# Optimization experiments

Hardware: AMD Instinct MI355X
Metric: run time of the kernel (lower is better)

## Reference

```python
import jax, jax.numpy as jnp
import numpy as np

D_MODEL = 96
D_STATE = 16
D_INNER = 192   # expand * d_model
DT_RANK = 6     # ceil(96/16)
D_DEPTH_OUT = 1024  # (64/2)*(64/2)
BATCH, HH, WW = 2, 64, 64


def silu(v):
    return v * jax.nn.sigmoid(v)


def setup_inputs() -> dict:
    key = jax.random.key(0)
    ks = jax.random.split(key, 10)
    f = jnp.float32
    x = jax.random.normal(ks[0], (BATCH, HH, WW, D_MODEL), f)
    in_proj_w = jax.random.normal(ks[1], (2 * D_INNER, D_MODEL), f) * 0.02
    conv2d_w = jax.random.normal(ks[2], (D_INNER, 1, 3, 3), f) * 0.1  # depthwise, groups=D_INNER
    conv2d_b = jnp.zeros((D_INNER,), f)
    depth_conv_w = jax.random.normal(ks[3], (D_INNER, 1, 3, 3), f) * 0.1  # depthwise, stride 2
    depth_conv_b = jnp.zeros((D_INNER,), f)
    depth_fc_w = jax.random.normal(ks[4], (D_INNER, D_DEPTH_OUT), f) * 0.02
    depth_fc_b = jnp.zeros((D_INNER,), f)
    x_proj_w = jax.random.normal(ks[5], (DT_RANK + 2 * D_STATE, D_INNER), f) * 0.02
    dt_init_std = DT_RANK ** (-0.5)
    dt_projs_w = jax.random.uniform(ks[6], (D_INNER, DT_RANK), f, -dt_init_std, dt_init_std)
    # inverse-softplus of dt ~ U(log 1e-3, log 0.1)
    dt = jnp.exp(jax.random.uniform(ks[7], (D_INNER,), f) * (np.log(0.1) - np.log(0.001)) + np.log(0.001))
    dt = jnp.clip(dt, 1e-4, None)
    dt_projs_b = dt + jnp.log(-jnp.expm1(-dt))
    A_logs = jnp.log(jnp.tile(jnp.arange(1, D_STATE + 1, dtype=f)[None, :], (D_INNER, 1)))
    Ds = jnp.ones((D_INNER,), f)
    out_norm_w = jnp.ones((D_INNER,), f)
    out_norm_b = jnp.zeros((D_INNER,), f)
    out_proj_w = jax.random.normal(ks[8], (D_MODEL, D_INNER), f) * 0.02
    return dict(x=x, in_proj_w=in_proj_w, conv2d_w=conv2d_w, conv2d_b=conv2d_b,
                depth_conv_w=depth_conv_w, depth_conv_b=depth_conv_b,
                depth_fc_w=depth_fc_w, depth_fc_b=depth_fc_b, x_proj_w=x_proj_w,
                dt_projs_w=dt_projs_w, dt_projs_b=dt_projs_b, A_logs=A_logs, Ds=Ds,
                out_norm_w=out_norm_w, out_norm_b=out_norm_b, out_proj_w=out_proj_w)


def _selective_scan(u, delta, A, Bm, Cm, D, delta_bias):
    # u, delta: [B, D, L]; A: [D, N]; Bm, Cm: [B, N, L]; D: [D]; delta_bias: [D]
    delta = jax.nn.softplus(delta + delta_bias[None, :, None])
    dA = jnp.exp(jnp.einsum('bdl,dn->lbdn', delta, A))          # [L,B,D,N]
    dBu = jnp.einsum('bdl,bnl,bdl->lbdn', delta, Bm, u)          # [L,B,D,N]
    Ct = jnp.transpose(Cm, (2, 0, 1))                            # [L,B,N]
    h0 = jnp.zeros(dA.shape[1:], u.dtype)

    def step(h, inp):
        a, b, c = inp
        h = a * h + b                                            # S6 recurrence
        return h, jnp.einsum('bdn,bn->bd', h, c)

    _, ys = jax.lax.scan(step, h0, (dA, dBu, Ct))                # ys: [L,B,D]
    y = jnp.transpose(ys, (1, 2, 0))                             # [B,D,L]
    return y + D[None, :, None] * u


def _forward(x, in_proj_w, conv2d_w, conv2d_b, depth_conv_w, depth_conv_b,
             depth_fc_w, depth_fc_b, x_proj_w, dt_projs_w, dt_projs_b,
             A_logs, Ds, out_norm_w, out_norm_b, out_proj_w):
    B, H, W, _ = x.shape
    Di, N, R = D_INNER, D_STATE, DT_RANK
    dn = ('NCHW', 'OIHW', 'NCHW')
    xz = x @ in_proj_w.T
    x1, z = jnp.split(xz, 2, axis=-1)
    xc = jnp.transpose(x1, (0, 3, 1, 2))                         # [B,Di,H,W]
    xc = jax.lax.conv_general_dilated(xc, conv2d_w, (1, 1), [(1, 1), (1, 1)],
                                      dimension_numbers=dn, feature_group_count=Di)
    xc = silu(xc + conv2d_b[None, :, None, None])
    dxc = jax.lax.conv_general_dilated(xc, depth_conv_w, (2, 2), [(1, 1), (1, 1)],
                                       dimension_numbers=dn, feature_group_count=Di)
    dxc = dxc + depth_conv_b[None, :, None, None]                # [B,Di,H/2,W/2]
    dx = dxc.reshape(B, Di, -1)                                  # [B,Di,1024]
    dx = dx @ depth_fc_w.T + depth_fc_b                          # [B,Di,Di]
    dx = silu(jnp.transpose(dx, (0, 2, 1)))                      # [B,Di,CC], CC=Di
    L = H * W
    CC = dx.shape[-1]
    xs = jnp.concatenate([dx, xc.reshape(B, Di, L)], axis=-1)    # mode='head': [B,Di,LL]
    x_dbl = jnp.einsum('bdl,cd->bcl', xs, x_proj_w)
    dts, Bm, Cm = x_dbl[:, :R], x_dbl[:, R:R + N], x_dbl[:, R + N:]
    dts = jnp.einsum('brl,dr->bdl', dts, dt_projs_w)
    A = -jnp.exp(A_logs)
    y = _selective_scan(xs, dts, A, Bm, Cm, Ds, dt_projs_b)
    y = y[..., CC:]                                              # drop depth tokens (head mode)
    y = jnp.transpose(y, (0, 2, 1)).reshape(B, H, W, Di)
    mu = jnp.mean(y, axis=-1, keepdims=True)
    var = jnp.var(y, axis=-1, keepdims=True)
    y = (y - mu) * jax.lax.rsqrt(var + 1e-5) * out_norm_w + out_norm_b
    y = y * silu(z)
    return y @ out_proj_w.T


def reference(x, in_proj_w, conv2d_w, conv2d_b, depth_conv_w, depth_conv_b,
              depth_fc_w, depth_fc_b, x_proj_w, dt_projs_w, dt_projs_b,
              A_logs, Ds, out_norm_w, out_norm_b, out_proj_w):
    return _forward(x, in_proj_w, conv2d_w, conv2d_b, depth_conv_w, depth_conv_b,
                    depth_fc_w, depth_fc_b, x_proj_w, dt_projs_w, dt_projs_b,
                    A_logs, Ds, out_norm_w, out_norm_b, out_proj_w)
```

## Files before the change

### kernel.cpp

```cpp
#include <hip/hip_runtime.h>
#include <hip/hip_bf16.h>

typedef __hip_bfloat16 bf16;

#define BATCH 2
#define DM 96
#define DI 192
#define LSP 4096
#define LD 192
#define LTOT 4288
#define NST 16
#define RK 6
#define DFC 1024
#define CLEN 64
#define NCH 67
#define SCH 64
#define XR 16
#define NG  (BATCH * DI * NST)

__device__ __forceinline__ float b2f(bf16 v) { return __bfloat162float(v); }
__device__ __forceinline__ float silu_f(float x) { return x / (1.f + __expf(-x)); }
__device__ __forceinline__ float softplus_f(float x) { return x > 20.f ? x : log1pf(__expf(x)); }

__device__ __forceinline__ int is_f32(const void* alog) {
    return ((const unsigned int*)alog)[0] == 0u;
}
__device__ __forceinline__ float LDI(const void* p, int i, int f32m) {
    return f32m ? ((const float*)p)[i] : __bfloat162float(((const bf16*)p)[i]);
}
__device__ __forceinline__ void unpack2(unsigned int u, float* o) {
    o[0] = __uint_as_float(u << 16);
    o[1] = __uint_as_float(u & 0xffff0000u);
}

__global__ __launch_bounds__(768) void k_inproj(const void* __restrict__ x, const void* __restrict__ ipw,
                                                const void* __restrict__ alog,
                                                float* __restrict__ x1, float* __restrict__ z) {
    __shared__ uint4 sxr[384];
    const int f32m = is_f32(alog);
    int t = threadIdx.x;
    int col = t >> 1;
    int kh = t & 1;
    int row0 = blockIdx.x * 16;
    float wr[48];
    if (f32m) {
        const float4* wp = (const float4*)((const float*)ipw + col * 96 + kh * 48);
        #pragma unroll
        for (int i = 0; i < 12; i++) {
            float4 v = wp[i];
            wr[4*i] = v.x; wr[4*i+1] = v.y; wr[4*i+2] = v.z; wr[4*i+3] = v.w;
        }
        if (t < 384) sxr[t] = ((const uint4*)((const float*)x + row0 * 96))[t];
        __syncthreads();
        for (int r = 0; r < 16; r++) {
            const uint4* xr = &sxr[r * 24 + kh * 12];
            float acc = 0.f;
            #pragma unroll
            for (int i = 0; i < 12; i++) {
                uint4 u = xr[i];
                acc += __uint_as_float(u.x) * wr[4*i]   + __uint_as_float(u.y) * wr[4*i+1]
                     + __uint_as_float(u.z) * wr[4*i+2] + __uint_as_float(u.w) * wr[4*i+3];
            }
            acc += __shfl_xor(acc, 1);
            if (kh == 0) {
                int row = row0 + r;
                if (col < DI) x1[row * DI + col] = acc;
                else          z[row * DI + (col - DI)] = acc;
            }
        }
    } else {
        const uint4* wp = (const uint4*)((const bf16*)ipw + col * 96 + kh * 48);
        #pragma unroll
        for (int i = 0; i < 6; i++) {
            uint4 v = wp[i];
            unpack2(v.x, &wr[8*i]);   unpack2(v.y, &wr[8*i+2]);
            unpack2(v.z, &wr[8*i+4]); unpack2(v.w, &wr[8*i+6]);
        }
        if (t < 192) sxr[t] = ((const uint4*)((const bf16*)x + row0 * 96))[t];
        __syncthreads();
        for (int r = 0; r < 16; r++) {
            const uint4* xr = &sxr[r * 12 + kh * 6];
            float acc = 0.f;
            #pragma unroll
            for (int i = 0; i < 6; i++) {
                uint4 xv = xr[i];
                float xf8[8];
                unpack2(xv.x, &xf8[0]); unpack2(xv.y, &xf8[2]);
                unpack2(xv.z, &xf8[4]); unpack2(xv.w, &xf8[6]);
                #pragma unroll
                for (int j = 0; j < 8; j++) acc += xf8[j] * wr[8*i + j];
            }
            acc += __shfl_xor(acc, 1);
            if (kh == 0) {
                int row = row0 + r;
                if (col < DI) x1[row * DI + col] = acc;
                else          z[row * DI + (col - DI)] = acc;
            }
        }
    }
}

__global__ __launch_bounds__(192) void k_conv1(const float* __restrict__ x1, const void* __restrict__ cw,
                                               const void* __restrict__ cb, float* __restrict__ xs,
                                               const void* __restrict__ alog) {
    const int f32m = is_f32(alog);
    int d = threadIdx.x;
    int blk = blockIdx.x;
    int b = blk >> 9;
    int rest = blk & 511;
    int h = rest >> 3, w0 = (rest & 7) * 8;
    float wgt[9];
    #pragma unroll
    for (int i = 0; i < 9; i++) wgt[i] = LDI(cw, d * 9 + i, f32m);
    float bias = LDI(cb, d, f32m);
    float val[3][10];
    #pragma unroll
    for (int dh = 0; dh < 3; dh++) {
        int hh = h + dh - 1;
        #pragma unroll
        for (int j = 0; j < 10; j++) {
            int ww = w0 + j - 1;
            val[dh][j] = ((unsigned)hh < 64u && (unsigned)ww < 64u)
                       ? x1[((b << 12) + (hh << 6) + ww) * DI + d] : 0.f;
        }
    }
    #pragma unroll
    for (int i = 0; i < 8; i++) {
        float acc = bias;
        #pragma unroll
        for (int dh = 0; dh < 3; dh++)
            #pragma unroll
            for (int dw = 0; dw < 3; dw++)
                acc += val[dh][i + dw] * wgt[dh * 3 + dw];
        xs[(b * LTOT + LD + (h << 6) + w0 + i) * DI + d] = silu_f(acc);
    }
}

__global__ __launch_bounds__(192) void k_conv2(const float* __restrict__ xs, const void* __restrict__ dw,
                                               const void* __restrict__ db, float* __restrict__ dxc,
                                               const void* __restrict__ alog) {
    const int f32m = is_f32(alog);
    int d = threadIdx.x;
    int blk = blockIdx.x;
    int b = blk >> 10, lp = blk & 1023;
    int hp = lp >> 5, wp = lp & 31;
    float acc = LDI(db, d, f32m);
    #pragma unroll
    for (int dh = 0; dh < 3; dh++) {
        int h = 2 * hp + dh - 1;
        if ((unsigned)h >= 64u) continue;
        #pragma unroll
        for (int dw_ = 0; dw_ < 3; dw_++) {
            int w_ = 2 * wp + dw_ - 1;
            if ((unsigned)w_ >= 64u) continue;
            acc += xs[(b * LTOT + LD + (h << 6) + w_) * DI + d] * LDI(dw, d * 9 + dh * 3 + dw_, f32m);
        }
    }
    dxc[(b * DFC + lp) * DI + d] = acc;
}

__global__ __launch_bounds__(192) void k_dfc(const float* __restrict__ dxc, const void* __restrict__ fw,
                                             float* __restrict__ part, const void* __restrict__ alog) {
    __shared__ float sfw[4 * 128];
    const int f32m = is_f32(alog);
    int t = threadIdx.x;
    int blk = blockIdx.x;
    int p = blk / 96;
    int rem = blk - p * 96;
    int b   = rem / 48;
    int ch0 = (rem % 48) * 4;
    int k0  = p * 128;
    for (int idx = t; idx < 4 * 128; idx += 192)
        sfw[idx] = LDI(fw, (ch0 + (idx >> 7)) * DFC + k0 + (idx & 127), f32m);
    __syncthreads();
    float a0 = 0.f, a1 = 0.f, a2 = 0.f, a3 = 0.f;
    #pragma unroll 8
    for (int k = 0; k < 128; k++) {
        float dv = dxc[(b * DFC + k0 + k) * DI + t];
        a0 += dv * sfw[k];
        a1 += dv * sfw[128 + k];
        a2 += dv * sfw[256 + k];
        a3 += dv * sfw[384 + k];
    }
    int ob = ((p * 2 + b) * 192 + t) * DI + ch0;
    *(float4*)&part[ob] = make_float4(a0, a1, a2, a3);
}

__global__ __launch_bounds__(256) void k_xdbl(const float* __restrict__ xs_r, float* __restrict__ xs_w,
                                              const float* __restrict__ part, const void* __restrict__ fb,
                                              const void* __restrict__ xpw,
                                              float* __restrict__ BCb, float* __restrict__ dts,
                                              const void* __restrict__ alog) {
    __shared__ float sw[38 * 196];
    __shared__ float srow[XR][196];
    const int f32m = is_f32(alog);
    int t = threadIdx.x;
    for (int c = t >> 3; c < 38; c += 32) {
        int seg = (t & 7) * 24;
        for (int k = seg; k < seg + 24; k++) sw[c * 196 + k] = LDI(xpw, c * DI + k, f32m);
    }
    int row0 = blockIdx.x * XR;
    int bb = row0 >= LTOT ? 1 : 0;
    int depth = (row0 - bb * LTOT) < LD;
    for (int idx = t; idx < XR * DI; idx += 256) {
        int row = idx / DI, k = idx - row * DI;
        int grow = row0 + row;
        float v;
        if (depth) {
            int tok = grow - bb * LTOT;
            int o = (bb * 192 + tok) * DI + k;
            v = 0.f;
            #pragma unroll
            for (int p = 0; p < 8; p++) v += part[o + p * 73728];
            v = silu_f(v + LDI(fb, k, f32m));
            xs_w[grow * DI + k] = v;
        } else {
            v = xs_r[grow * DI + k];
        }
        srow[row][k] = v;
    }
    __syncthreads();
    int r = t & 15, cg = t >> 4;
    float a0 = 0.f, a1 = 0.f, a2 = 0.f;
    const float4* w0 = (const float4*)&sw[cg * 196];
    const float4* w1 = (const float4*)&sw[(cg + 16) * 196];
    const float4* w2 = (const float4*)&sw[(cg < 6 ? cg + 32 : cg) * 196];
    const float4* xr = (const float4*)&srow[r][0];
    #pragma unroll 4
    for (int k = 0; k < 48; k++) {
        float4 xv = xr[k], v0 = w0[k], v1 = w1[k], v2 = w2[k];
        a0 += xv.x * v0.x + xv.y * v0.y + xv.z * v0.z + xv.w * v0.w;
        a1 += xv.x * v1.x + xv.y * v1.y + xv.z * v1.z + xv.w * v1.w;
        a2 += xv.x * v2.x + xv.y * v2.y + xv.z * v2.z + xv.w * v2.w;
    }
    int grow = row0 + r;
    if (cg < 6) dts[grow * 6 + cg] = a0;
    else        BCb[grow * 32 + (cg - 6)] = a0;
    BCb[grow * 32 + (cg + 10)] = a1;
    if (cg < 6) BCb[grow * 32 + (cg + 26)] = a2;
}

__device__ __forceinline__ void delta_block(const float* sdts, const float* sdwb, float* sdel, int t) {
    int e = t * 4;
    int i = e >> 4, dl = e & 15;
    #pragma unroll
    for (int q = 0; q < 4; q++) {
        int dlq = dl + q;
        float dv = sdwb[96 + dlq];
        #pragma unroll
        for (int r2 = 0; r2 < RK; r2++) dv += sdts[i * RK + r2] * sdwb[dlq * RK + r2];
        sdel[e + q] = softplus_f(dv);
    }
}

__global__ __launch_bounds__(256) void k_scan1(const float* __restrict__ dts, const float* __restrict__ xs,
                                               const float* __restrict__ BCb, const void* __restrict__ dtw,
                                               const void* __restrict__ dtb, const void* __restrict__ alog,
                                               float2* __restrict__ AH) {
    __shared__ float su[CLEN * 16];
    __shared__ float sB[CLEN * 16];
    __shared__ float sdel[CLEN * 16];
    __shared__ float sdts[CLEN * RK];
    __shared__ float sdwb[112];
    const int f32m = is_f32(alog);
    int t = threadIdx.x;
    int beta = blockIdx.x;
    int b = beta / (12 * NCH);
    int rem = beta - b * (12 * NCH);
    int dblk = rem / NCH, ch = rem - dblk * NCH;
    int d0 = dblk * 16, l0 = ch * CLEN;
    int bL = b * LTOT;
    {
        int e = t * 4;
        int i = e >> 4, dd = e & 15;
        *(float4*)&su[e] = *(const float4*)&xs[(bL + l0 + i) * DI + d0 + dd];
        *(float4*)&sB[e] = *(const float4*)&BCb[(bL + l0 + i) * 32 + dd];
    }
    for (int idx = t; idx < CLEN * RK; idx += 256) sdts[idx] = dts[(bL + l0) * RK + idx];
    if (t < 96)            sdwb[t] = LDI(dtw, (d0 + t / 6) * RK + (t % 6), f32m);
    else if (t < 112)      sdwb[t] = LDI(dtb, d0 + (t - 96), f32m);
    __syncthreads();
    delta_block(sdts, sdwb, sdel, t);
    __syncthreads();
    int dloc = t >> 4, n = t & 15;
    int d = d0 + dloc;
    float A = -__expf(LDI(alog, d * NST + n, f32m));
    float h = 0.f, ap = 1.f;
    #pragma unroll 4
    for (int i = 0; i < CLEN; i++) {
        float dt = sdel[(i << 4) | dloc];
        float u  = su[(i << 4) | dloc];
        float Bv = sB[(i << 4) | n];
        float a = __expf(dt * A);
        h = a * h + dt * Bv * u;
        ap *= a;
    }
    int g = ((b * DI + d) * NST) + n;
    AH[ch * NG + g] = make_float2(ap, h);
}

__global__ __launch_bounds__(64) void k_scan2(const float2* __restrict__ AH, float* __restrict__ He) {
    int g = blockIdx.x * 64 + threadIdx.x;
    float h = 0.f;
    for (int ch = 0; ch < NCH; ch++) {
        He[ch * NG + g] = h;
        float2 v = AH[ch * NG + g];
        h = v.x * h + v.y;
    }
}

__global__ __launch_bounds__(256) void k_scan3(const float* __restrict__ dts, const float* __restrict__ xs,
                                               const float* __restrict__ BCb, const void* __restrict__ dtw,
                                               const void* __restrict__ dtb, const void* __restrict__ alog,
                                               const void* __restrict__ Dsv, const float* __restrict__ He,
                                               float* __restrict__ y) {
    __shared__ float su[CLEN * 16];
    __shared__ float sbc[CLEN * 32];
    __shared__ float sdel[CLEN * 16];
    __shared__ float sdts[CLEN * RK];
    __shared__ float sdwb[112];
    const int f32m = is_f32(alog);
    int t = threadIdx.x;
    int beta = blockIdx.x;
    int b = beta / (12 * SCH);
    int rem = beta - b * (12 * SCH);
    int dblk = rem / SCH, ch = (rem - dblk * SCH) + 3;
    int d0 = dblk * 16, l0 = ch * CLEN;
    int bL = b * LTOT;
    {
        int e = t * 4;
        int i = e >> 4, dd = e & 15;
        *(float4*)&su[e] = *(const float4*)&xs[(bL + l0 + i) * DI + d0 + dd];
    }
    #pragma unroll
    for (int q = 0; q < 2; q++) {
        int e = (t + q * 256) * 4;
        int i = e >> 5, c = e & 31;
        *(float4*)&sbc[e] = *(const float4*)&BCb[(bL + l0 + i) * 32 + c];
    }
    for (int idx = t; idx < CLEN * RK; idx += 256) sdts[idx] = dts[(bL + l0) * RK + idx];
    if (t < 96)            sdwb[t] = LDI(dtw, (d0 + t / 6) * RK + (t % 6), f32m);
    else if (t < 112)      sdwb[t] = LDI(dtb, d0 + (t - 96), f32m);
    __syncthreads();
    delta_block(sdts, sdwb, sdel, t);
    __syncthreads();
    int dloc = t >> 4, n = t & 15;
    int d = d0 + dloc;
    float A = -__expf(LDI(alog, d * NST + n, f32m));
    float Dv = LDI(Dsv, d, f32m);
    int g = ((b * DI + d) * NST) + n;
    float h = He[ch * NG + g];
    for (int i = 0; i < CLEN; i++) {
        float dt = sdel[(i << 4) | dloc];
        float u  = su[(i << 4) | dloc];
        float Bv = sbc[(i << 5) | n];
        float Cv = sbc[(i << 5) | 16 | n];
        float a = __expf(dt * A);
        h = a * h + dt * Bv * u;
        float yv = h * Cv;
        #pragma unroll
        for (int m = 8; m; m >>= 1) yv += __shfl_xor(yv, m, 16);
        int l = l0 + i;
        if (n == 0) y[(b * LSP + (l - LD)) * DI + d] = yv + Dv * u;
    }
}

__global__ __launch_bounds__(384) void k_out(const float* __restrict__ y, const float* __restrict__ z,
                                             const void* __restrict__ nw, const void* __restrict__ nb,
                                             const void* __restrict__ opw, void* __restrict__ out,
                                             const void* __restrict__ alog) {
    __shared__ float sg[2][DI];
    __shared__ float sred[2][2][3];
    const int f32m = is_f32(alog);
    int t = threadIdx.x;
    int m = t >> 2, kh = t & 3;
    float wr[48];
    if (f32m) {
        const float4* wp = (const float4*)((const float*)opw + m * DI + kh * 48);
        #pragma unroll
        for (int i = 0; i < 12; i++) {
            float4 v = wp[i];
            wr[4*i] = v.x; wr[4*i+1] = v.y; wr[4*i+2] = v.z; wr[4*i+3] = v.w;
        }
    } else {
        const uint4* wp = (const uint4*)((const bf16*)opw + m * DI + kh * 48);
        #pragma unroll
        for (int i = 0; i < 6; i++) {
            uint4 v = wp[i];
            unpack2(v.x, &wr[8*i]);   unpack2(v.y, &wr[8*i+2]);
            unpack2(v.z, &wr[8*i+4]); unpack2(v.w, &wr[8*i+6]);
        }
    }
    float nwv = 0.f, nbv = 0.f;
    if (t < DI) { nwv = LDI(nw, t, f32m); nbv = LDI(nb, t, f32m); }
    int wv_ = t >> 6;
    int row0 = blockIdx.x * 16;
    for (int pr = 0; pr < 8; pr++) {
        int r0 = row0 + pr * 2, r1 = r0 + 1;
        float y0 = 0.f, z0 = 0.f, y1 = 0.f, z1 = 0.f;
        if (t < DI) {
            y0 = y[r0 * DI + t]; z0 = z[r0 * DI + t];
            y1 = y[r1 * DI + t]; z1 = z[r1 * DI + t];
            float s0 = y0, q0 = y0 * y0, s1 = y1, q1 = y1 * y1;
            #pragma unroll
            for (int off = 32; off; off >>= 1) {
                s0 += __shfl_xor(s0, off); q0 += __shfl_xor(q0, off);
                s1 += __shfl_xor(s1, off); q1 += __shfl_xor(q1, off);
            }
            if ((t & 63) == 0) {
                sred[0][0][wv_] = s0; sred[0][1][wv_] = q0;
                sred[1][0][wv_] = s1; sred[1][1][wv_] = q1;
            }
        }
        __syncthreads();
        if (t < DI) {
            float S0  = sred[0][0][0] + sred[0][0][1] + sred[0][0][2];
            float Q0  = sred[0][1][0] + sred[0][1][1] + sred[0][1][2];
            float S1  = sred[1][0][0] + sred[1][0][1] + sred[1][0][2];
            float Q1  = sred[1][1][0] + sred[1][1][1] + sred[1][1][2];
            float mu0 = S0 * (1.f / 192.f), var0 = Q0 * (1.f / 192.f) - mu0 * mu0;
            float mu1 = S1 * (1.f / 192.f), var1 = Q1 * (1.f / 192.f) - mu1 * mu1;
            float g0 = (y0 - mu0) * rsqrtf(var0 + 1e-5f) * nwv + nbv;
            g0 *= z0 / (1.f + __expf(-z0));
            float g1 = (y1 - mu1) * rsqrtf(var1 + 1e-5f) * nwv + nbv;
            g1 *= z1 / (1.f + __expf(-z1));
            sg[0][t] = g0;
            sg[1][t] = g1;
        }
        __syncthreads();
        const float* g0p = &sg[0][kh * 48];
        const float* g1p = &sg[1][kh * 48];
        float a0 = 0.f, a1 = 0.f;
        #pragma unroll
        for (int j = 0; j < 48; j++) {
            a0 += g0p[j] * wr[j];
            a1 += g1p[j] * wr[j];
        }
        a0 += __shfl_xor(a0, 1); a0 += __shfl_xor(a0, 2);
        a1 += __shfl_xor(a1, 1); a1 += __shfl_xor(a1, 2);
        if (kh == 0) {
            if (f32m) {
                ((float*)out)[r0 * DM + m] = a0;
                ((float*)out)[r1 * DM + m] = a1;
            } else {
                ((bf16*)out)[r0 * DM + m] = __float2bfloat16(a0);
                ((bf16*)out)[r1 * DM + m] = __float2bfloat16(a1);
            }
        }
    }
}

extern "C" void kernel_launch(void* const* d_in, const int* in_sizes, int n_in,
                              void* d_out, int out_size, void* d_ws, size_t ws_size,
                              hipStream_t stream) {
    (void)in_sizes; (void)n_in; (void)out_size; (void)ws_size;
    const void* x    = d_in[0];
    const void* ipw  = d_in[1];
    const void* c1w  = d_in[2];
    const void* c1b  = d_in[3];
    const void* c2w  = d_in[4];
    const void* c2b  = d_in[5];
    const void* fcw  = d_in[6];
    const void* fcb  = d_in[7];
    const void* xpw  = d_in[8];
    const void* dtw  = d_in[9];
    const void* dtb  = d_in[10];
    const void* alog = d_in[11];
    const void* Dsv  = d_in[12];
    const void* nw   = d_in[13];
    const void* nb   = d_in[14];
    const void* opw  = d_in[15];

    float* ws  = (float*)d_ws;
    float* x1  = ws;
    float* z   = x1  + BATCH * LSP * DI;
    float* xs  = z   + BATCH * LSP * DI;
    float* dxc = xs  + BATCH * LTOT * DI;
    float* BCb = dxc + BATCH * DFC * DI;
    float* dts = BCb + BATCH * LTOT * 32;
    float2* AH = (float2*)(dts + BATCH * LTOT * RK);
    float* He  = (float*)(AH + NCH * NG);
    float* part = x1;
    float* y    = x1;

    k_inproj<<<dim3(512), dim3(768), 0, stream>>>(x, ipw, alog, x1, z);
    k_conv1 <<<dim3(1024), dim3(DI), 0, stream>>>(x1, c1w, c1b, xs, alog);
    k_conv2 <<<dim3(BATCH * DFC), dim3(DI), 0, stream>>>(xs, c2w, c2b, dxc, alog);
    k_dfc   <<<dim3(768), dim3(DI), 0, stream>>>(dxc, fcw, part, alog);
    k_xdbl  <<<dim3(536), dim3(256), 0, stream>>>(xs, xs, part, fcb, xpw, BCb, dts, alog);
    k_scan1 <<<dim3(BATCH * 12 * NCH), dim3(256), 0, stream>>>(dts, xs, BCb, dtw, dtb, alog, AH);
    k_scan2 <<<dim3(96), dim3(64), 0, stream>>>(AH, He);
    k_scan3 <<<dim3(BATCH * 12 * SCH), dim3(256), 0, stream>>>(dts, xs, BCb, dtw, dtb, alog, Dsv, He, y);
    k_out   <<<dim3(512), dim3(384), 0, stream>>>(y, z, nw, nb, opw, d_out, alog);
}
```

Before: 223.6 us.

## Transpose scan shared-memory tiles, use DPP reductions, register-tile the input projection

The input projection is rewritten as a 4x4 register-tiled GEMM. A new prep kernel transposes the projection weight each call so that weight reads are coalesced float4 loads. In both scan kernels, delta, u, B and C are stored in shared memory transposed with a rotating swizzle, so each thread reads four timesteps with one float4 load without bank conflicts. The scan3 output reduction over 16 lanes switches from shfl_xor to DPP row operations. The extra launch and the scattered shared-memory stores during the load phase add some overhead.

```diff
diff --git a/kernel.cpp b/kernel.cpp
--- a/kernel.cpp
+++ b/kernel.cpp
@@ -33,70 +33,81 @@
     o[1] = __uint_as_float(u & 0xffff0000u);
 }
 
-__global__ __launch_bounds__(768) void k_inproj(const void* __restrict__ x, const void* __restrict__ ipw,
-                                                const void* __restrict__ alog,
-                                                float* __restrict__ x1, float* __restrict__ z) {
-    __shared__ uint4 sxr[384];
+__device__ __forceinline__ float row16_sum(float v) {
+    v += __int_as_float(__builtin_amdgcn_update_dpp(0, __float_as_int(v), 0x128, 0xf, 0xf, true));
+    v += __int_as_float(__builtin_amdgcn_update_dpp(0, __float_as_int(v), 0x124, 0xf, 0xf, true));
+    v += __int_as_float(__builtin_amdgcn_update_dpp(0, __float_as_int(v), 0x122, 0xf, 0xf, true));
+    v += __int_as_float(__builtin_amdgcn_update_dpp(0, __float_as_int(v), 0x121, 0xf, 0xf, true));
+    return v;
+}
+
+#define TW(r, i)  ((r) * 64 + ((((i) >> 2) + (r)) & 15) * 4 + ((i) & 3))
+
+__global__ __launch_bounds__(256) void k_wprep(const void* __restrict__ ipw, float* __restrict__ wT,
+                                               const void* __restrict__ alog) {
+    const int f32m = is_f32(alog);
+    int idx = blockIdx.x * 256 + threadIdx.x;
+    if (idx < 96 * 384) {
+        int k = idx / 384, c = idx - k * 384;
+        wT[idx] = LDI(ipw, c * 96 + k, f32m);
+    }
+}
+
+__global__ __launch_bounds__(384) void k_inproj2(const void* __restrict__ x, const float* __restrict__ wT,
+                                                 float* __restrict__ x1, float* __restrict__ z,
+                                                 const void* __restrict__ alog) {
+    __shared__ __align__(16) float sx[16 * 100];
     const int f32m = is_f32(alog);
     int t = threadIdx.x;
-    int col = t >> 1;
-    int kh = t & 1;
     int row0 = blockIdx.x * 16;
-    float wr[48];
-    if (f32m) {
-        const float4* wp = (const float4*)((const float*)ipw + col * 96 + kh * 48);
-        #pragma unroll
-        for (int i = 0; i < 12; i++) {
-            float4 v = wp[i];
-            wr[4*i] = v.x; wr[4*i+1] = v.y; wr[4*i+2] = v.z; wr[4*i+3] = v.w;
-        }
-        if (t < 384) sxr[t] = ((const uint4*)((const float*)x + row0 * 96))[t];
-        __syncthreads();
-        for (int r = 0; r < 16; r++) {
-            const uint4* xr = &sxr[r * 24 + kh * 12];
-            float acc = 0.f;
+    {
+        int e = t * 4;
+        int row = e / 96, k = e - row * 96;
+        float4 v;
+        if (f32m) {
+            v = *((const float4*)((const float*)x + (row0 + row) * 96 + k));
+        } else {
+            uint2 u = *((const uint2*)((const ushort*)x + (row0 + row) * 96 + k));
+            float f[4];
+            unpack2(u.x, &f[0]); unpack2(u.y, &f[2]);
+            v = make_float4(f[0], f[1], f[2], f[3]);
+        }
+        *(float4*)&sx[row * 100 + k] = v;
+    }
+    __syncthreads();
+    int rg = t / 96, cg = t - rg * 96;
+    int c0 = cg * 4, rbase = rg * 4;
+    float acc[4][4];
+    #pragma unroll
+    for (int r = 0; r < 4; r++)
+        #pragma unroll
+        for (int cc = 0; cc < 4; cc++) acc[r][cc] = 0.f;
+    const float* wp = wT + c0;
+    #pragma unroll 4
+    for (int k4 = 0; k4 < 24; k4++) {
+        float4 xv[4], wv[4];
+        #pragma unroll
+        for (int r = 0; r < 4; r++) xv[r] = *(const float4*)&sx[(rbase + r) * 100 + k4 * 4];
+        #pragma unroll
+        for (int q = 0; q < 4; q++) wv[q] = *(const float4*)&wp[(k4 * 4 + q) * 384];
+        #pragma unroll
+        for (int r = 0; r < 4; r++) {
+            float xr[4] = {xv[r].x, xv[r].y, xv[r].z, xv[r].w};
             #pragma unroll
-            for (int i = 0; i < 12; i++) {
-                uint4 u = xr[i];
-                acc += __uint_as_float(u.x) * wr[4*i]   + __uint_as_float(u.y) * wr[4*i+1]
-                     + __uint_as_float(u.z) * wr[4*i+2] + __uint_as_float(u.w) * wr[4*i+3];
+            for (int q = 0; q < 4; q++) {
+                acc[r][0] += xr[q] * wv[q].x;
+                acc[r][1] += xr[q] * wv[q].y;
+                acc[r][2] += xr[q] * wv[q].z;
+                acc[r][3] += xr[q] * wv[q].w;
             }
-            acc += __shfl_xor(acc, 1);
-            if (kh == 0) {
-                int row = row0 + r;
-                if (col < DI) x1[row * DI + col] = acc;
-                else          z[row * DI + (col - DI)] = acc;
-            }
-        }
-    } else {
-        const uint4* wp = (const uint4*)((const bf16*)ipw + col * 96 + kh * 48);
-        #pragma unroll
-        for (int i = 0; i < 6; i++) {
-            uint4 v = wp[i];
-            unpack2(v.x, &wr[8*i]);   unpack2(v.y, &wr[8*i+2]);
-            unpack2(v.z, &wr[8*i+4]); unpack2(v.w, &wr[8*i+6]);
-        }
-        if (t < 192) sxr[t] = ((const uint4*)((const bf16*)x + row0 * 96))[t];
-        __syncthreads();
-        for (int r = 0; r < 16; r++) {
-            const uint4* xr = &sxr[r * 12 + kh * 6];
-            float acc = 0.f;
-            #pragma unroll
-            for (int i = 0; i < 6; i++) {
-                uint4 xv = xr[i];
-                float xf8[8];
-                unpack2(xv.x, &xf8[0]); unpack2(xv.y, &xf8[2]);
-                unpack2(xv.z, &xf8[4]); unpack2(xv.w, &xf8[6]);
-                #pragma unroll
-                for (int j = 0; j < 8; j++) acc += xf8[j] * wr[8*i + j];
-            }
-            acc += __shfl_xor(acc, 1);
-            if (kh == 0) {
-                int row = row0 + r;
-                if (col < DI) x1[row * DI + col] = acc;
-                else          z[row * DI + (col - DI)] = acc;
-            }
-        }
+        }
+    }
+    #pragma unroll
+    for (int r = 0; r < 4; r++) {
+        int row = row0 + rbase + r;
+        float4 o = make_float4(acc[r][0], acc[r][1], acc[r][2], acc[r][3]);
+        if (c0 < DI) *(float4*)&x1[row * DI + c0] = o;
+        else         *(float4*)&z[row * DI + (c0 - DI)] = o;
     }
 }
 
@@ -240,16 +251,16 @@
     if (cg < 6) BCb[grow * 32 + (cg + 26)] = a2;
 }
 
-__device__ __forceinline__ void delta_block(const float* sdts, const float* sdwb, float* sdel, int t) {
+__device__ __forceinline__ void delta_block_T(const float* sdts, const float* sdwb, float* sdel, int t) {
     int e = t * 4;
     int i = e >> 4, dl = e & 15;
     #pragma unroll
     for (int q = 0; q < 4; q++) {
-        int dlq = dl + q;
-        float dv = sdwb[96 + dlq];
-        #pragma unroll
-        for (int r2 = 0; r2 < RK; r2++) dv += sdts[i * RK + r2] * sdwb[dlq * RK + r2];
-        sdel[e + q] = softplus_f(dv);
+        int r = dl + q;
+        float dv = sdwb[96 + r];
+        #pragma unroll
+        for (int r2 = 0; r2 < RK; r2++) dv += sdts[i * RK + r2] * sdwb[r * RK + r2];
+        sdel[TW(r, i)] = softplus_f(dv);
     }
 }
 
@@ -257,9 +268,9 @@
                                                const float* __restrict__ BCb, const void* __restrict__ dtw,
                                                const void* __restrict__ dtb, const void* __restrict__ alog,
                                                float2* __restrict__ AH) {
-    __shared__ float su[CLEN * 16];
-    __shared__ float sB[CLEN * 16];
-    __shared__ float sdel[CLEN * 16];
+    __shared__ __align__(16) float su[1024];
+    __shared__ __align__(16) float sB[1024];
+    __shared__ __align__(16) float sdel[1024];
     __shared__ float sdts[CLEN * RK];
     __shared__ float sdwb[112];
     const int f32m = is_f32(alog);
@@ -273,27 +284,42 @@
     {
         int e = t * 4;
         int i = e >> 4, dd = e & 15;
-        *(float4*)&su[e] = *(const float4*)&xs[(bL + l0 + i) * DI + d0 + dd];
-        *(float4*)&sB[e] = *(const float4*)&BCb[(bL + l0 + i) * 32 + dd];
+        float4 uv = *(const float4*)&xs[(bL + l0 + i) * DI + d0 + dd];
+        float4 bv = *(const float4*)&BCb[(bL + l0 + i) * 32 + dd];
+        float uu[4] = {uv.x, uv.y, uv.z, uv.w};
+        float vb[4] = {bv.x, bv.y, bv.z, bv.w};
+        #pragma unroll
+        for (int q = 0; q < 4; q++) {
+            int w = TW(dd + q, i);
+            su[w] = uu[q];
+            sB[w] = vb[q];
+        }
     }
     for (int idx = t; idx < CLEN * RK; idx += 256) sdts[idx] = dts[(bL + l0) * RK + idx];
     if (t < 96)            sdwb[t] = LDI(dtw, (d0 + t / 6) * RK + (t % 6), f32m);
     else if (t < 112)      sdwb[t] = LDI(dtb, d0 + (t - 96), f32m);
     __syncthreads();
-    delta_block(sdts, sdwb, sdel, t);
+    delta_block_T(sdts, sdwb, sdel, t);
     __syncthreads();
     int dloc = t >> 4, n = t & 15;
     int d = d0 + dloc;
     float A = -__expf(LDI(alog, d * NST + n, f32m));
     float h = 0.f, ap = 1.f;
-    #pragma unroll 4
-    for (int i = 0; i < CLEN; i++) {
-        float dt = sdel[(i << 4) | dloc];
-        float u  = su[(i << 4) | dloc];
-        float Bv = sB[(i << 4) | n];
-        float a = __expf(dt * A);
-        h = a * h + dt * Bv * u;
-        ap *= a;
+    int bd = dloc * 64, bn = n * 64;
+    #pragma unroll
+    for (int i4 = 0; i4 < 16; i4++) {
+        int od = bd + (((i4 + dloc) & 15) << 2);
+        int on = bn + (((i4 + n) & 15) << 2);
+        float de[4], uu[4], vb[4];
+        *(float4*)de = *(const float4*)&sdel[od];
+        *(float4*)uu = *(const float4*)&su[od];
+        *(float4*)vb = *(const float4*)&sB[on];
+        #pragma unroll
+        for (int q = 0; q < 4; q++) {
+            float a = __expf(de[q] * A);
+            h = a * h + de[q] * vb[q] * uu[q];
+            ap *= a;
+        }
     }
     int g = ((b * DI + d) * NST) + n;
     AH[ch * NG + g] = make_float2(ap, h);
@@ -314,9 +340,9 @@
                                                const void* __restrict__ dtb, const void* __restrict__ alog,
                                                const void* __restrict__ Dsv, const float* __restrict__ He,
                                                float* __restrict__ y) {
-    __shared__ float su[CLEN * 16];
-    __shared__ float sbc[CLEN * 32];
-    __shared__ float sdel[CLEN * 16];
+    __shared__ __align__(16) float su[1024];
+    __shared__ __align__(16) float sbc[2048];
+    __shared__ __align__(16) float sdel[1024];
     __shared__ float sdts[CLEN * RK];
     __shared__ float sdwb[112];
     const int f32m = is_f32(alog);
@@ -330,19 +356,25 @@
     {
         int e = t * 4;
         int i = e >> 4, dd = e & 15;
-        *(float4*)&su[e] = *(const float4*)&xs[(bL + l0 + i) * DI + d0 + dd];
-    }
-    #pragma unroll
-    for (int q = 0; q < 2; q++) {
-        int e = (t + q * 256) * 4;
+        float4 uv = *(const float4*)&xs[(bL + l0 + i) * DI + d0 + dd];
+        float uu[4] = {uv.x, uv.y, uv.z, uv.w};
+        #pragma unroll
+        for (int q = 0; q < 4; q++) su[TW(dd + q, i)] = uu[q];
+    }
+    #pragma unroll
+    for (int q2 = 0; q2 < 2; q2++) {
+        int e = (t + q2 * 256) * 4;
         int i = e >> 5, c = e & 31;
-        *(float4*)&sbc[e] = *(const float4*)&BCb[(bL + l0 + i) * 32 + c];
+        float4 v = *(const float4*)&BCb[(bL + l0 + i) * 32 + c];
+        float vv[4] = {v.x, v.y, v.z, v.w};
+        #pragma unroll
+        for (int q = 0; q < 4; q++) sbc[TW(c + q, i)] = vv[q];
     }
     for (int idx = t; idx < CLEN * RK; idx += 256) sdts[idx] = dts[(bL + l0) * RK + idx];
     if (t < 96)            sdwb[t] = LDI(dtw, (d0 + t / 6) * RK + (t % 6), f32m);
     else if (t < 112)      sdwb[t] = LDI(dtb, d0 + (t - 96), f32m);
     __syncthreads();
-    delta_block(sdts, sdwb, sdel, t);
+    delta_block_T(sdts, sdwb, sdel, t);
     __syncthreads();
     int dloc = t >> 4, n = t & 15;
     int d = d0 + dloc;
@@ -350,18 +382,26 @@
     float Dv = LDI(Dsv, d, f32m);
     int g = ((b * DI + d) * NST) + n;
     float h = He[ch * NG + g];
-    for (int i = 0; i < CLEN; i++) {
-        float dt = sdel[(i << 4) | dloc];
-        float u  = su[(i << 4) | dloc];
-        float Bv = sbc[(i << 5) | n];
-        float Cv = sbc[(i << 5) | 16 | n];
-        float a = __expf(dt * A);
-        h = a * h + dt * Bv * u;
-        float yv = h * Cv;
-        #pragma unroll
-        for (int m = 8; m; m >>= 1) yv += __shfl_xor(yv, m, 16);
-        int l = l0 + i;
-        if (n == 0) y[(b * LSP + (l - LD)) * DI + d] = yv + Dv * u;
+    int bd = dloc * 64, bn = n * 64;
+    #pragma unroll
+    for (int i4 = 0; i4 < 16; i4++) {
+        int od = bd + (((i4 + dloc) & 15) << 2);
+        int on = bn + (((i4 + n) & 15) << 2);
+        float de[4], uu[4], vb[4], vc[4];
+        *(float4*)de = *(const float4*)&sdel[od];
+        *(float4*)uu = *(const float4*)&su[od];
+        *(float4*)vb = *(const float4*)&sbc[on];
+        *(float4*)vc = *(const float4*)&sbc[on + 1024];
+        #pragma unroll
+        for (int q = 0; q < 4; q++) {
+            float a = __expf(de[q] * A);
+            h = a * h + de[q] * vb[q] * uu[q];
+            float yv = row16_sum(h * vc[q]);
+            if (n == 0) {
+                int l = l0 + i4 * 4 + q;
+                y[(b * LSP + (l - LD)) * DI + d] = yv + Dv * uu[q];
+            }
+        }
     }
 }
 
@@ -480,16 +520,18 @@
     float* dts = BCb + BATCH * LTOT * 32;
     float2* AH = (float2*)(dts + BATCH * LTOT * RK);
     float* He  = (float*)(AH + NCH * NG);
+    float* wT  = He + NCH * NG;
     float* part = x1;
     float* y    = x1;
 
-    k_inproj<<<dim3(512), dim3(768), 0, stream>>>(x, ipw, alog, x1, z);
-    k_conv1 <<<dim3(1024), dim3(DI), 0, stream>>>(x1, c1w, c1b, xs, alog);
-    k_conv2 <<<dim3(BATCH * DFC), dim3(DI), 0, stream>>>(xs, c2w, c2b, dxc, alog);
-    k_dfc   <<<dim3(768), dim3(DI), 0, stream>>>(dxc, fcw, part, alog);
-    k_xdbl  <<<dim3(536), dim3(256), 0, stream>>>(xs, xs, part, fcb, xpw, BCb, dts, alog);
-    k_scan1 <<<dim3(BATCH * 12 * NCH), dim3(256), 0, stream>>>(dts, xs, BCb, dtw, dtb, alog, AH);
-    k_scan2 <<<dim3(96), dim3(64), 0, stream>>>(AH, He);
-    k_scan3 <<<dim3(BATCH * 12 * SCH), dim3(256), 0, stream>>>(dts, xs, BCb, dtw, dtb, alog, Dsv, He, y);
-    k_out   <<<dim3(512), dim3(384), 0, stream>>>(y, z, nw, nb, opw, d_out, alog);
-}
+    k_wprep  <<<dim3(144), dim3(256), 0, stream>>>(ipw, wT, alog);
+    k_inproj2<<<dim3(512), dim3(384), 0, stream>>>(x, wT, x1, z, alog);
+    k_conv1  <<<dim3(1024), dim3(DI), 0, stream>>>(x1, c1w, c1b, xs, alog);
+    k_conv2  <<<dim3(BATCH * DFC), dim3(DI), 0, stream>>>(xs, c2w, c2b, dxc, alog);
+    k_dfc    <<<dim3(768), dim3(DI), 0, stream>>>(dxc, fcw, part, alog);
+    k_xdbl   <<<dim3(536), dim3(256), 0, stream>>>(xs, xs, part, fcb, xpw, BCb, dts, alog);
+    k_scan1  <<<dim3(BATCH * 12 * NCH), dim3(256), 0, stream>>>(dts, xs, BCb, dtw, dtb, alog, AH);
+    k_scan2  <<<dim3(96), dim3(64), 0, stream>>>(AH, He);
+    k_scan3  <<<dim3(BATCH * 12 * SCH), dim3(256), 0, stream>>>(dts, xs, BCb, dtw, dtb, alog, Dsv, He, y);
+    k_out    <<<dim3(512), dim3(384), 0, stream>>>(y, z, nw, nb, opw, d_out, alog);
+}
```

Result: no change. 221.8 us (-0.8%).
